# Kernel optimization log

Measured on AMD Instinct MI355X. Metric: run time of the kernel, lower is better.

Reference implementation:

```python
import jax, jax.numpy as jnp
import numpy as np

DIM = 128
HEADS = 8
HD = DIM // HEADS          # head_dim = 16
KD = HD // 2               # key_dim = 8 (attn_ratio=0.5)
EPS = 1e-3                 # BatchNorm eps
SCALE = KD ** -0.5


def _bn(x, g, b, m, v):
    # eval-mode BatchNorm2d over channel axis (NCHW)
    s = (g / jnp.sqrt(v + EPS))[None, :, None, None]
    return (x - m[None, :, None, None]) * s + b[None, :, None, None]


def _conv1x1(x, w):
    # w: [Cout, Cin, 1, 1]
    return jnp.einsum('oi,bihw->bohw', w[:, :, 0, 0], x)


def _dwconv3(x, w):
    # depthwise 3x3, pad 1; w: [C, 1, 3, 3]
    return jax.lax.conv_general_dilated(
        x, w, window_strides=(1, 1), padding=((1, 1), (1, 1)),
        feature_group_count=x.shape[1],
        dimension_numbers=('NCHW', 'OIHW', 'NCHW'))


def setup_inputs() -> dict:
    key = jax.random.key(0)
    ks = jax.random.split(key, 20)
    H_CH = DIM + 2 * KD * HEADS  # 256
    x = jax.random.normal(ks[0], (4, DIM, 40, 40), dtype=jnp.float32)

    def bn_params(k, c):
        k1, k2, k3, k4 = jax.random.split(k, 4)
        g = 1.0 + 0.1 * jax.random.normal(k1, (c,), jnp.float32)
        b = 0.1 * jax.random.normal(k2, (c,), jnp.float32)
        m = 0.1 * jax.random.normal(k3, (c,), jnp.float32)
        v = jax.random.uniform(k4, (c,), jnp.float32, 0.5, 1.5)
        return g, b, m, v

    qkv_w = 0.05 * jax.random.normal(ks[1], (H_CH, DIM, 1, 1), jnp.float32)
    qkv_g, qkv_b, qkv_m, qkv_v = bn_params(ks[2], H_CH)
    pe_w = 0.05 * jax.random.normal(ks[3], (DIM, 1, 3, 3), jnp.float32)
    pe_g, pe_b, pe_m, pe_v = bn_params(ks[4], DIM)
    proj_w = 0.05 * jax.random.normal(ks[5], (DIM, DIM, 1, 1), jnp.float32)
    proj_g, proj_b, proj_m, proj_v = bn_params(ks[6], DIM)

    return dict(x=x,
                qkv_w=qkv_w, qkv_g=qkv_g, qkv_b=qkv_b, qkv_m=qkv_m, qkv_v=qkv_v,
                pe_w=pe_w, pe_g=pe_g, pe_b=pe_b, pe_m=pe_m, pe_v=pe_v,
                proj_w=proj_w, proj_g=proj_g, proj_b=proj_b, proj_m=proj_m, proj_v=proj_v)


def reference(x, qkv_w, qkv_g, qkv_b, qkv_m, qkv_v,
              pe_w, pe_g, pe_b, pe_m, pe_v,
              proj_w, proj_g, proj_b, proj_m, proj_v):
    b, c, H, W = x.shape
    n = H * W
    qkv = _bn(_conv1x1(x, qkv_w), qkv_g, qkv_b, qkv_m, qkv_v)
    qkv = qkv.reshape(b, HEADS, 2 * KD + HD, n)
    q, k, v = qkv[:, :, :KD], qkv[:, :, KD:2 * KD], qkv[:, :, 2 * KD:]
    # attn[b,h,n,m] = sum_k q[b,h,k,n] * k[b,h,k,m] * scale
    attn = jnp.einsum('bhkn,bhkm->bhnm', q, k) * SCALE
    attn = jax.nn.softmax(attn, axis=-1)
    # out = v @ attn^T : [b,h,hd,n]
    out = jnp.einsum('bhdn,bhmn->bhdm', v, attn).reshape(b, c, H, W)
    pe = _bn(_dwconv3(v.reshape(b, c, H, W), pe_w), pe_g, pe_b, pe_m, pe_v)
    y = _bn(_conv1x1(out + pe, proj_w), proj_g, proj_b, proj_m, proj_v)
    return y
```

## Files before the change

### kernel.cpp

```cpp
#include <hip/hip_runtime.h>
#include <hip/hip_bf16.h>

#define NB 4
#define CDIM 128
#define NPIX 1600
#define WIMG 40
#define HCH 256
#define NHEADS 8
#define KDQ 8
#define HDV 16
#define EPSV 1e-3f
#define SCALEV 0.35355339059327373f
#define KT 320
#define KLP 24
#define VTP (KT + 8)

typedef unsigned short u16;
typedef float f32x4 __attribute__((ext_vector_type(4)));
typedef __bf16 bf16x8 __attribute__((ext_vector_type(8)));

union U16B { uint4 u; bf16x8 v; };

__device__ __forceinline__ u16 f2bf(float f) {
  unsigned u = __float_as_uint(f);
  return (u16)((u + 0x7FFFu + ((u >> 16) & 1u)) >> 16);
}
__device__ __forceinline__ float bf2f(u16 b) {
  return __uint_as_float(((unsigned)b) << 16);
}
__device__ __forceinline__ unsigned cvt_pk_bf16(float lo, float hi) {
  unsigned r;
  asm("v_cvt_pk_bf16_f32 %0, %1, %2" : "=v"(r) : "v"(lo), "v"(hi));
  return r;
}

__global__ __launch_bounds__(512) void k_qkv(
    const float* __restrict__ x, const float* __restrict__ w,
    const float* __restrict__ gg, const float* __restrict__ bb,
    const float* __restrict__ mm, const float* __restrict__ vv,
    float* __restrict__ vf32, u16* __restrict__ qbf,
    u16* __restrict__ kbf, u16* __restrict__ vtbf)
{
  const int pblk = blockIdx.x % 7;
  const int ct   = (blockIdx.x / 7) % (HCH / 8);
  const int b    = blockIdx.x / (7 * (HCH / 8));
  const int tid  = threadIdx.x;
  const int half = tid >> 8;
  const int t    = tid & 255;

  __shared__ float wl[8][CDIM];
  __shared__ float red[256][8];
  for (int i = tid; i < 8 * CDIM; i += 512)
    wl[i >> 7][i & 127] = w[(ct * 8 + (i >> 7)) * CDIM + (i & 127)];
  __syncthreads();

  const int praw = pblk * 256 + t;
  const int p    = praw < NPIX ? praw : NPIX - 1;

  const float* xb = x + (size_t)b * CDIM * NPIX + p;
  float acc[8] = {0.f, 0.f, 0.f, 0.f, 0.f, 0.f, 0.f, 0.f};
  const int c0 = half * 64;
#pragma unroll 4
  for (int ci = c0; ci < c0 + 64; ++ci) {
    const float xv = xb[(size_t)ci * NPIX];
#pragma unroll
    for (int j = 0; j < 8; ++j) acc[j] += wl[j][ci] * xv;
  }

  if (half == 1) {
#pragma unroll
    for (int j = 0; j < 8; ++j) red[t][j] = acc[j];
  }
  __syncthreads();
  if (half == 1 || praw >= NPIX) return;
#pragma unroll
  for (int j = 0; j < 8; ++j) acc[j] += red[t][j];

  const int grp = ct & 3;
  const int h   = ct >> 2;
  float o[8];
#pragma unroll
  for (int j = 0; j < 8; ++j) {
    const int c = ct * 8 + j;
    const float sc = gg[c] * rsqrtf(vv[c] + EPSV);
    const float bi = bb[c] - mm[c] * sc;
    o[j] = acc[j] * sc + bi;
    if (grp == 0) o[j] *= SCALEV;
  }

  if (grp <= 1) {
    u16 hb[8], lb[8];
#pragma unroll
    for (int j = 0; j < 8; ++j) {
      hb[j] = f2bf(o[j]);
      lb[j] = f2bf(o[j] - bf2f(hb[j]));
    }
    uint4 H, L;
    H.x = hb[0] | ((unsigned)hb[1] << 16);
    H.y = hb[2] | ((unsigned)hb[3] << 16);
    H.z = hb[4] | ((unsigned)hb[5] << 16);
    H.w = hb[6] | ((unsigned)hb[7] << 16);
    L.x = lb[0] | ((unsigned)lb[1] << 16);
    L.y = lb[2] | ((unsigned)lb[3] << 16);
    L.z = lb[4] | ((unsigned)lb[5] << 16);
    L.w = lb[6] | ((unsigned)lb[7] << 16);
    u16* dst = (grp == 0) ? qbf : kbf;
    const size_t base = ((size_t)(b * NHEADS + h) * NPIX + p) * 16;
    *(uint4*)&dst[base]     = H;
    *(uint4*)&dst[base + 8] = L;
  } else {
    const int d0 = (grp == 2) ? 0 : 8;
#pragma unroll
    for (int j = 0; j < 8; ++j) {
      vtbf[((size_t)(b * NHEADS + h) * HDV + d0 + j) * NPIX + p] = f2bf(o[j]);
      vf32[((size_t)b * CDIM + h * HDV + d0 + j) * NPIX + p] = o[j];
    }
  }
}

__global__ __launch_bounds__(512) void k_attn(
    const u16* __restrict__ qbf, const u16* __restrict__ kbf,
    const u16* __restrict__ vtbf, const float* __restrict__ vf32,
    const float* __restrict__ pw, const float* __restrict__ pg,
    const float* __restrict__ pbb, const float* __restrict__ pm,
    const float* __restrict__ pv, float* __restrict__ atb)
{
  const int bh   = blockIdx.x & 31;
  const int qblk = blockIdx.x >> 5;
  const int b = bh >> 3, h = bh & 7;
  const int tid = threadIdx.x;
  const int lane = tid & 63, wid = tid >> 6;
  const int qw = wid & 3, kh = wid >> 2;
  const int qloc = lane & 15, g = lane >> 4;

  __shared__ __align__(16) u16 Klds[KT][KLP];
  __shared__ __align__(16) u16 Vtlds[HDV][VTP];
  __shared__ float red[256][6];

  const int qglob = qblk * 64 + qw * 16 + qloc;
  U16B qf;
  qf.u = *(const uint4*)&qbf[((size_t)bh * NPIX + qglob) * 16 + (g & 1) * 8];

  f32x4 c3 = {0.f, 0.f, 0.f, 0.f};
  float lsum = 0.f;
  const int idx0 = (((g & 1) << 5) | qloc) << 2;
  const int idx1 = idx0 + 64;
  const bool selA = (g < 2);
  const f32x4 zf = {0.f, 0.f, 0.f, 0.f};
  const int ksel = (g >> 1) * 8;

  for (int kt = 0; kt < NPIX / KT; ++kt) {
    const int kb0 = kt * KT;
    __syncthreads();
    for (int i = tid; i < KT * 2; i += 512) {
      const int r = i >> 1, hf = (i & 1) * 8;
      *(uint4*)&Klds[r][hf] =
          *(const uint4*)&kbf[((size_t)bh * NPIX + kb0 + r) * 16 + hf];
    }
    for (int c = tid; c < HDV * (KT / 8); c += 512) {
      const int d = c / (KT / 8), n0 = (c % (KT / 8)) * 8;
      *(uint4*)&Vtlds[d][n0] =
          *(const uint4*)&vtbf[((size_t)bh * HDV + d) * NPIX + kb0 + n0];
    }
    __syncthreads();

    for (int ks = kh * 5; ks < kh * 5 + 5; ++ks) {
      U16B kfA, kfB;
      kfA.u = *(const uint4*)&Klds[ks * 32 + qloc][ksel];
      kfB.u = *(const uint4*)&Klds[ks * 32 + 16 + qloc][ksel];
      f32x4 cA = __builtin_amdgcn_mfma_f32_16x16x32_bf16(kfA.v, qf.v, zf, 0, 0, 0);
      f32x4 cB = __builtin_amdgcn_mfma_f32_16x16x32_bf16(kfB.v, qf.v, zf, 0, 0, 0);

      const unsigned pkA0 = cvt_pk_bf16(__expf(cA[0]), __expf(cA[1]));
      const unsigned pkA1 = cvt_pk_bf16(__expf(cA[2]), __expf(cA[3]));
      const unsigned pkB0 = cvt_pk_bf16(__expf(cB[0]), __expf(cB[1]));
      const unsigned pkB1 = cvt_pk_bf16(__expf(cB[2]), __expf(cB[3]));

      const int a0 = __builtin_amdgcn_ds_bpermute(idx0, (int)pkA0);
      const int b0 = __builtin_amdgcn_ds_bpermute(idx0, (int)pkB0);
      const int a1 = __builtin_amdgcn_ds_bpermute(idx0, (int)pkA1);
      const int b1 = __builtin_amdgcn_ds_bpermute(idx0, (int)pkB1);
      const int a2 = __builtin_amdgcn_ds_bpermute(idx1, (int)pkA0);
      const int b2 = __builtin_amdgcn_ds_bpermute(idx1, (int)pkB0);
      const int a3 = __builtin_amdgcn_ds_bpermute(idx1, (int)pkA1);
      const int b3 = __builtin_amdgcn_ds_bpermute(idx1, (int)pkB1);
      U16B pf;
      pf.u.x = (unsigned)(selA ? a0 : b0);
      pf.u.y = (unsigned)(selA ? a1 : b1);
      pf.u.z = (unsigned)(selA ? a2 : b2);
      pf.u.w = (unsigned)(selA ? a3 : b3);

      lsum += __uint_as_float(pf.u.x << 16) + __uint_as_float(pf.u.x & 0xFFFF0000u)
            + __uint_as_float(pf.u.y << 16) + __uint_as_float(pf.u.y & 0xFFFF0000u)
            + __uint_as_float(pf.u.z << 16) + __uint_as_float(pf.u.z & 0xFFFF0000u)
            + __uint_as_float(pf.u.w << 16) + __uint_as_float(pf.u.w & 0xFFFF0000u);

      U16B vf4;
      vf4.u = *(const uint4*)&Vtlds[qloc][ks * 32 + g * 8];

      c3 = __builtin_amdgcn_mfma_f32_16x16x32_bf16(vf4.v, pf.v, c3, 0, 0, 0);
    }
  }

  if (kh == 1) {
    const int rr = qw * 64 + lane;
    red[rr][0] = c3[0]; red[rr][1] = c3[1];
    red[rr][2] = c3[2]; red[rr][3] = c3[3];
    red[rr][4] = lsum;
  }
  __syncthreads();
  if (kh == 1) return;
  {
    const int rr = qw * 64 + lane;
    c3[0] += red[rr][0]; c3[1] += red[rr][1];
    c3[2] += red[rr][2]; c3[3] += red[rr][3];
    lsum  += red[rr][4];
  }

  lsum += __shfl_xor(lsum, 16);
  lsum += __shfl_xor(lsum, 32);
  const float rl = 1.f / lsum;

  const int p  = qblk * 64 + qw * 16 + qloc;
  const int yy = p / WIMG, xx = p % WIMG;
  const float* vb = vf32 + ((size_t)b * CDIM + h * HDV) * NPIX;
  float* ob = atb + ((size_t)b * CDIM + h * HDV) * NPIX + p;
#pragma unroll
  for (int r = 0; r < 4; ++r) {
    const int d = g * 4 + r;
    const int c = h * HDV + d;
    float acc = 0.f;
#pragma unroll
    for (int dy = -1; dy <= 1; ++dy)
#pragma unroll
      for (int dx = -1; dx <= 1; ++dx) {
        const int y2 = yy + dy, x2 = xx + dx;
        if ((unsigned)y2 < (unsigned)WIMG && (unsigned)x2 < (unsigned)WIMG)
          acc += pw[c * 9 + (dy + 1) * 3 + (dx + 1)] * vb[(size_t)d * NPIX + y2 * WIMG + x2];
      }
    const float sc = pg[c] * rsqrtf(pv[c] + EPSV);
    const float bi = pbb[c] - pm[c] * sc;
    ob[(size_t)d * NPIX] = c3[r] * rl + acc * sc + bi;
  }
}

__global__ __launch_bounds__(256) void k_proj(
    const float* __restrict__ atb, const float* __restrict__ w,
    const float* __restrict__ gg, const float* __restrict__ bb,
    const float* __restrict__ mm, const float* __restrict__ vv,
    float* __restrict__ out)
{
  const int pblk = blockIdx.x % 7;
  const int ct   = (blockIdx.x / 7) % (CDIM / 2);
  const int b    = blockIdx.x / (7 * (CDIM / 2));
  const int tid  = threadIdx.x;

  __shared__ float wl[2][CDIM];
  wl[tid >> 7][tid & 127] = w[(ct * 2 + (tid >> 7)) * CDIM + (tid & 127)];
  __syncthreads();

  const int p = pblk * 256 + tid;
  if (p >= NPIX) return;

  const float* ab = atb + (size_t)b * CDIM * NPIX + p;
  float a0 = 0.f, a1 = 0.f;
#pragma unroll 8
  for (int ci = 0; ci < CDIM; ++ci) {
    const float xv = ab[(size_t)ci * NPIX];
    a0 += wl[0][ci] * xv;
    a1 += wl[1][ci] * xv;
  }
#pragma unroll
  for (int j = 0; j < 2; ++j) {
    const int c = ct * 2 + j;
    const float sc = gg[c] * rsqrtf(vv[c] + EPSV);
    const float bi = bb[c] - mm[c] * sc;
    out[((size_t)b * CDIM + c) * NPIX + p] = (j ? a1 : a0) * sc + bi;
  }
}

extern "C" void kernel_launch(void* const* d_in, const int* in_sizes, int n_in,
                              void* d_out, int out_size, void* d_ws, size_t ws_size,
                              hipStream_t stream)
{
  const float* x      = (const float*)d_in[0];
  const float* qkv_w  = (const float*)d_in[1];
  const float* qkv_g  = (const float*)d_in[2];
  const float* qkv_b  = (const float*)d_in[3];
  const float* qkv_m  = (const float*)d_in[4];
  const float* qkv_v  = (const float*)d_in[5];
  const float* pe_w   = (const float*)d_in[6];
  const float* pe_g   = (const float*)d_in[7];
  const float* pe_b   = (const float*)d_in[8];
  const float* pe_m   = (const float*)d_in[9];
  const float* pe_v   = (const float*)d_in[10];
  const float* proj_w = (const float*)d_in[11];
  const float* proj_g = (const float*)d_in[12];
  const float* proj_b = (const float*)d_in[13];
  const float* proj_m = (const float*)d_in[14];
  const float* proj_v = (const float*)d_in[15];

  float* ws   = (float*)d_ws;
  float* vf32 = ws;
  float* atb  = vf32 + (size_t)NB * CDIM * NPIX;
  u16*   qbf  = (u16*)(atb + (size_t)NB * CDIM * NPIX);
  u16*   kbf  = qbf + (size_t)NB * NHEADS * NPIX * 16;
  u16*   vtbf = kbf + (size_t)NB * NHEADS * NPIX * 16;

  k_qkv<<<dim3(NB * (HCH / 8) * 7), 512, 0, stream>>>(
      x, qkv_w, qkv_g, qkv_b, qkv_m, qkv_v, vf32, qbf, kbf, vtbf);
  k_attn<<<dim3(NB * NHEADS * 25), 512, 0, stream>>>(
      qbf, kbf, vtbf, vf32, pe_w, pe_g, pe_b, pe_m, pe_v, atb);
  k_proj<<<dim3(NB * (CDIM / 2) * 7), 256, 0, stream>>>(
      atb, proj_w, proj_g, proj_b, proj_m, proj_v, (float*)d_out);
}
```

Baseline: 145.7 us.

## Load K/V fragments directly from global memory in attention, drop LDS staging

The attention kernel no longer stages K and V^T tiles in shared memory behind block-wide barriers. Each wave now reads its MFMA operand fragments straight from global (L2/L1-cached) memory across its half of the keys. This removes two __syncthreads per tile and the LDS traffic, at the cost of redundant global loads across the four query waves and possible exposed load latency. Unroll factors in the two 1x1 conv kernels are also raised.

```diff
diff --git a/kernel.cpp b/kernel.cpp
--- a/kernel.cpp
+++ b/kernel.cpp
@@ -11,9 +11,6 @@
 #define HDV 16
 #define EPSV 1e-3f
 #define SCALEV 0.35355339059327373f
-#define KT 320
-#define KLP 24
-#define VTP (KT + 8)
 
 typedef unsigned short u16;
 typedef float f32x4 __attribute__((ext_vector_type(4)));
@@ -60,7 +57,7 @@
   const float* xb = x + (size_t)b * CDIM * NPIX + p;
   float acc[8] = {0.f, 0.f, 0.f, 0.f, 0.f, 0.f, 0.f, 0.f};
   const int c0 = half * 64;
-#pragma unroll 4
+#pragma unroll 8
   for (int ci = c0; ci < c0 + 64; ++ci) {
     const float xv = xb[(size_t)ci * NPIX];
 #pragma unroll
@@ -133,9 +130,7 @@
   const int qw = wid & 3, kh = wid >> 2;
   const int qloc = lane & 15, g = lane >> 4;
 
-  __shared__ __align__(16) u16 Klds[KT][KLP];
-  __shared__ __align__(16) u16 Vtlds[HDV][VTP];
-  __shared__ float red[256][6];
+  __shared__ float red[256][5];
 
   const int qglob = qblk * 64 + qw * 16 + qloc;
   U16B qf;
@@ -149,57 +144,44 @@
   const f32x4 zf = {0.f, 0.f, 0.f, 0.f};
   const int ksel = (g >> 1) * 8;
 
-  for (int kt = 0; kt < NPIX / KT; ++kt) {
-    const int kb0 = kt * KT;
-    __syncthreads();
-    for (int i = tid; i < KT * 2; i += 512) {
-      const int r = i >> 1, hf = (i & 1) * 8;
-      *(uint4*)&Klds[r][hf] =
-          *(const uint4*)&kbf[((size_t)bh * NPIX + kb0 + r) * 16 + hf];
-    }
-    for (int c = tid; c < HDV * (KT / 8); c += 512) {
-      const int d = c / (KT / 8), n0 = (c % (KT / 8)) * 8;
-      *(uint4*)&Vtlds[d][n0] =
-          *(const uint4*)&vtbf[((size_t)bh * HDV + d) * NPIX + kb0 + n0];
-    }
-    __syncthreads();
-
-    for (int ks = kh * 5; ks < kh * 5 + 5; ++ks) {
-      U16B kfA, kfB;
-      kfA.u = *(const uint4*)&Klds[ks * 32 + qloc][ksel];
-      kfB.u = *(const uint4*)&Klds[ks * 32 + 16 + qloc][ksel];
-      f32x4 cA = __builtin_amdgcn_mfma_f32_16x16x32_bf16(kfA.v, qf.v, zf, 0, 0, 0);
-      f32x4 cB = __builtin_amdgcn_mfma_f32_16x16x32_bf16(kfB.v, qf.v, zf, 0, 0, 0);
-
-      const unsigned pkA0 = cvt_pk_bf16(__expf(cA[0]), __expf(cA[1]));
-      const unsigned pkA1 = cvt_pk_bf16(__expf(cA[2]), __expf(cA[3]));
-      const unsigned pkB0 = cvt_pk_bf16(__expf(cB[0]), __expf(cB[1]));
-      const unsigned pkB1 = cvt_pk_bf16(__expf(cB[2]), __expf(cB[3]));
-
-      const int a0 = __builtin_amdgcn_ds_bpermute(idx0, (int)pkA0);
-      const int b0 = __builtin_amdgcn_ds_bpermute(idx0, (int)pkB0);
-      const int a1 = __builtin_amdgcn_ds_bpermute(idx0, (int)pkA1);
-      const int b1 = __builtin_amdgcn_ds_bpermute(idx0, (int)pkB1);
-      const int a2 = __builtin_amdgcn_ds_bpermute(idx1, (int)pkA0);
-      const int b2 = __builtin_amdgcn_ds_bpermute(idx1, (int)pkB0);
-      const int a3 = __builtin_amdgcn_ds_bpermute(idx1, (int)pkA1);
-      const int b3 = __builtin_amdgcn_ds_bpermute(idx1, (int)pkB1);
-      U16B pf;
-      pf.u.x = (unsigned)(selA ? a0 : b0);
-      pf.u.y = (unsigned)(selA ? a1 : b1);
-      pf.u.z = (unsigned)(selA ? a2 : b2);
-      pf.u.w = (unsigned)(selA ? a3 : b3);
-
-      lsum += __uint_as_float(pf.u.x << 16) + __uint_as_float(pf.u.x & 0xFFFF0000u)
-            + __uint_as_float(pf.u.y << 16) + __uint_as_float(pf.u.y & 0xFFFF0000u)
-            + __uint_as_float(pf.u.z << 16) + __uint_as_float(pf.u.z & 0xFFFF0000u)
-            + __uint_as_float(pf.u.w << 16) + __uint_as_float(pf.u.w & 0xFFFF0000u);
-
-      U16B vf4;
-      vf4.u = *(const uint4*)&Vtlds[qloc][ks * 32 + g * 8];
-
-      c3 = __builtin_amdgcn_mfma_f32_16x16x32_bf16(vf4.v, pf.v, c3, 0, 0, 0);
-    }
+  const u16* kbase = kbf + (size_t)bh * NPIX * 16;
+  const u16* vbase = vtbf + ((size_t)bh * HDV + qloc) * NPIX;
+
+  for (int s = 0; s < 25; ++s) {
+    const int key0 = kh * 800 + s * 32;
+    U16B kfA, kfB, vf4;
+    kfA.u = *(const uint4*)&kbase[(size_t)(key0 + qloc) * 16 + ksel];
+    kfB.u = *(const uint4*)&kbase[(size_t)(key0 + 16 + qloc) * 16 + ksel];
+    vf4.u = *(const uint4*)&vbase[key0 + g * 8];
+
+    f32x4 cA = __builtin_amdgcn_mfma_f32_16x16x32_bf16(kfA.v, qf.v, zf, 0, 0, 0);
+    f32x4 cB = __builtin_amdgcn_mfma_f32_16x16x32_bf16(kfB.v, qf.v, zf, 0, 0, 0);
+
+    const unsigned pkA0 = cvt_pk_bf16(__expf(cA[0]), __expf(cA[1]));
+    const unsigned pkA1 = cvt_pk_bf16(__expf(cA[2]), __expf(cA[3]));
+    const unsigned pkB0 = cvt_pk_bf16(__expf(cB[0]), __expf(cB[1]));
+    const unsigned pkB1 = cvt_pk_bf16(__expf(cB[2]), __expf(cB[3]));
+
+    const int a0 = __builtin_amdgcn_ds_bpermute(idx0, (int)pkA0);
+    const int b0 = __builtin_amdgcn_ds_bpermute(idx0, (int)pkB0);
+    const int a1 = __builtin_amdgcn_ds_bpermute(idx0, (int)pkA1);
+    const int b1 = __builtin_amdgcn_ds_bpermute(idx0, (int)pkB1);
+    const int a2 = __builtin_amdgcn_ds_bpermute(idx1, (int)pkA0);
+    const int b2 = __builtin_amdgcn_ds_bpermute(idx1, (int)pkB0);
+    const int a3 = __builtin_amdgcn_ds_bpermute(idx1, (int)pkA1);
+    const int b3 = __builtin_amdgcn_ds_bpermute(idx1, (int)pkB1);
+    U16B pf;
+    pf.u.x = (unsigned)(selA ? a0 : b0);
+    pf.u.y = (unsigned)(selA ? a1 : b1);
+    pf.u.z = (unsigned)(selA ? a2 : b2);
+    pf.u.w = (unsigned)(selA ? a3 : b3);
+
+    lsum += __uint_as_float(pf.u.x << 16) + __uint_as_float(pf.u.x & 0xFFFF0000u)
+          + __uint_as_float(pf.u.y << 16) + __uint_as_float(pf.u.y & 0xFFFF0000u)
+          + __uint_as_float(pf.u.z << 16) + __uint_as_float(pf.u.z & 0xFFFF0000u)
+          + __uint_as_float(pf.u.w << 16) + __uint_as_float(pf.u.w & 0xFFFF0000u);
+
+    c3 = __builtin_amdgcn_mfma_f32_16x16x32_bf16(vf4.v, pf.v, c3, 0, 0, 0);
   }
 
   if (kh == 1) {
@@ -264,7 +246,7 @@
 
   const float* ab = atb + (size_t)b * CDIM * NPIX + p;
   float a0 = 0.f, a1 = 0.f;
-#pragma unroll 8
+#pragma unroll 16
   for (int ci = 0; ci < CDIM; ++ci) {
     const float xv = ab[(size_t)ci * NPIX];
     a0 += wl[0][ci] * xv;
```

Measured after the change: 152.5 us. +4.7%, slower.
